# Kernel tuning notes

Measured on AMD Instinct MI355X. Metric: run time of the kernel, lower is better.

The kernel has to match this reference:

```python
import jax, jax.numpy as jnp
import numpy as np

ALPHA = 0.2  # leaky_relu negative slope
NEG_INF = -9e15


def gat_layer(h_in, W, a, adj_mask):
    """One GATLayer (eval mode, dropout disabled).
    h_in: [N, F_in], W: [F_in, F_out], a: [2*F_out, 1], adj_mask: [N, N] bool.
    Equivalent to the torch repeat/cat construction: e_ij = leaky_relu(a1.h_i + a2.h_j).
    """
    h = h_in @ W                          # [N, F_out]
    F_out = W.shape[1]
    a1 = a[:F_out, 0]                     # [F_out]
    a2 = a[F_out:, 0]                     # [F_out]
    f1 = h @ a1                           # [N]
    f2 = h @ a2                           # [N]
    e = jax.nn.leaky_relu(f1[:, None] + f2[None, :], negative_slope=ALPHA)  # [N, N]
    e = jnp.where(adj_mask, e, NEG_INF)
    attn = jax.nn.softmax(e, axis=-1)     # rows sum to 1
    return jax.nn.elu(attn @ h)           # [N, F_out]


def setup_inputs() -> dict:
    key = jax.random.key(0)
    ks = jax.random.split(key, 6)
    N, F_in, F_hid, F_out, H = 8192, 29, 8, 2, 4
    x = jax.random.normal(ks[0], (N, F_in), dtype=jnp.float32)
    adj = jax.random.randint(ks[1], (N, N), 0, 2, dtype=jnp.int32)
    # xavier_uniform with gain=1.414
    def xavier(k, shape, gain=1.414):
        fan_in, fan_out = shape[0], shape[1]
        bound = gain * np.sqrt(6.0 / (fan_in + fan_out))
        return jax.random.uniform(k, shape, jnp.float32, -bound, bound)
    W_heads = jnp.stack([xavier(k, (F_in, F_hid)) for k in jax.random.split(ks[2], H)])   # [H, 29, 8]
    a_heads = jnp.stack([xavier(k, (2 * F_hid, 1)) for k in jax.random.split(ks[3], H)])  # [H, 16, 1]
    W_out = xavier(ks[4], (F_hid * H, F_out))   # [32, 2]
    a_out = xavier(ks[5], (2 * F_out, 1))       # [4, 1]
    return {"x": x, "adj": adj, "W_heads": W_heads, "a_heads": a_heads,
            "W_out": W_out, "a_out": a_out}


def reference(x, adj, W_heads, a_heads, W_out, a_out):
    adj_mask = adj > 0
    heads = jax.vmap(lambda W, a: gat_layer(x, W, a, adj_mask))(W_heads, a_heads)  # [H, N, 8]
    hcat = jnp.concatenate(list(heads), axis=1)   # [N, H*8] (same order as torch cat over heads)
    out = gat_layer(hcat, W_out, a_out, adj_mask)  # [N, 2]
    return jax.nn.log_softmax(out, axis=1)
```

## Files before the change

### kernel.cpp

```cpp
#include <hip/hip_runtime.h>
#include <math.h>

#define N 8192
#define NW 128
#define FIN 29
#define FH 8
#define NH 4
#define ALPHA 0.2f
#define LOG2E 1.4426950408889634f

typedef unsigned long long ull;

__device__ inline unsigned bf16rn(float f) {
    unsigned u = __float_as_uint(f);
    return (u + 0x7fffu + ((u >> 16) & 1u)) >> 16;
}
__device__ inline float2 bfpair(unsigned u) {
    return make_float2(__uint_as_float(u << 16), __uint_as_float(u & 0xffff0000u));
}
__device__ inline unsigned fenc(float x) {
    unsigned u = __float_as_uint(x);
    return (u & 0x80000000u) ? ~u : (u | 0x80000000u);
}
__device__ inline float fdec(unsigned e) {
    return __uint_as_float((e & 0x80000000u) ? (e & 0x7fffffffu) : ~e);
}

__global__ void k0_pack(const int* __restrict__ adj, ull* __restrict__ mask,
                        unsigned* __restrict__ amax) {
    int row = blockIdx.x;
    int tid = threadIdx.x;
    int lane = tid & 63;
    int wave = tid >> 6;
    if (row == 0 && tid < 8) amax[tid] = 0u;
    const int* rp = adj + (size_t)row * N;
#pragma unroll 8
    for (int i = 0; i < 32; i++) {
        int a = rp[i * 256 + tid];
        ull b = __ballot(a > 0);
        if (lane == 0) mask[(size_t)row * NW + i * 4 + wave] = b;
    }
}

__global__ __launch_bounds__(64) void k1_feat(
    const float* __restrict__ x, const float* __restrict__ Wh,
    const float* __restrict__ ah,
    float* __restrict__ f2p, uint4* __restrict__ hpk,
    float* __restrict__ f1a, unsigned* __restrict__ amax) {
    __shared__ float sW[NH * FIN * FH];
    __shared__ float sa[NH * 2 * FH];
    int tid = threadIdx.x;
    for (int i = tid; i < NH * FIN * FH; i += 64) sW[i] = Wh[i];
    for (int i = tid; i < NH * 2 * FH; i += 64) sa[i] = ah[i];
    __syncthreads();
    int node = blockIdx.x * 64 + tid;
    float xr[FIN];
#pragma unroll
    for (int f = 0; f < FIN; f++) xr[f] = x[node * FIN + f];
    float f2v[NH];
#pragma unroll
    for (int h = 0; h < NH; h++) {
        float hv[FH];
#pragma unroll
        for (int k = 0; k < FH; k++) {
            float s = 0.f;
#pragma unroll
            for (int f = 0; f < FIN; f++) s += xr[f] * sW[(h * FIN + f) * FH + k];
            hv[k] = s;
        }
        float f1 = 0.f, f2 = 0.f;
#pragma unroll
        for (int k = 0; k < FH; k++) {
            f1 += hv[k] * sa[h * 16 + k];
            f2 += hv[k] * sa[h * 16 + 8 + k];
        }
        f2v[h] = f2 * LOG2E;
        f2p[h * N + node] = f2v[h];
        f1a[node * 4 + h] = f1 * LOG2E;
        uint4 p;
        p.x = (bf16rn(hv[1]) << 16) | bf16rn(hv[0]);
        p.y = (bf16rn(hv[3]) << 16) | bf16rn(hv[2]);
        p.z = (bf16rn(hv[5]) << 16) | bf16rn(hv[4]);
        p.w = (bf16rn(hv[7]) << 16) | bf16rn(hv[6]);
        hpk[h * N + node] = p;
    }
#pragma unroll
    for (int h = 0; h < NH; h++) {
        float v = f2v[h];
        for (int off = 32; off > 0; off >>= 1) v = fmaxf(v, __shfl_xor(v, off, 64));
        if (tid == 0) atomicMax(&amax[h], fenc(v));
    }
}

#define TJ 512
#define JS1 2
__global__ __launch_bounds__(512) void k3_attn1(
    const ull* __restrict__ mask, const float* __restrict__ f2p,
    const uint4* __restrict__ hpk, const float* __restrict__ f1a,
    const unsigned* __restrict__ amax, float* __restrict__ part1) {
    __shared__ float tF2[TJ];
    __shared__ uint4 tH[TJ];
    int tid = threadIdx.x;
    int lane = tid & 63;
    int wave = tid >> 6;
    int h = blockIdx.x & 3;
    int js = (blockIdx.x >> 2) & (JS1 - 1);
    int rowblk = blockIdx.x >> 3;
    int r0 = rowblk * 16 + wave * 2;
    int r1 = r0 + 1;
    const int JR = N / JS1;
    int jbase = js * JR;

    float mf = fdec(amax[h]);
    float f1 = f1a[r0 * 4 + h];
    float v = f1 + mf, m = fmaxf(v, ALPHA * v);
    float f1m0 = f1 - m, f1q0 = ALPHA * f1 - m;
    f1 = f1a[r1 * 4 + h];
    v = f1 + mf; m = fmaxf(v, ALPHA * v);
    float f1m1 = f1 - m, f1q1 = ALPHA * f1 - m;

    float acc0[FH], acc1[FH], d0 = 0.f, d1 = 0.f;
#pragma unroll
    for (int k = 0; k < FH; k++) { acc0[k] = 0.f; acc1[k] = 0.f; }

    const ull* mr0 = mask + (size_t)r0 * NW;
    const ull* mr1 = mask + (size_t)r1 * NW;

    for (int t = 0; t < JR / TJ; t++) {
        __syncthreads();
        int gb = jbase + t * TJ + tid;
        tH[tid] = hpk[h * N + gb];
        tF2[tid] = f2p[h * N + gb];
        __syncthreads();
        int wb = (jbase >> 6) + t * (TJ / 64);
#pragma unroll
        for (int s = 0; s < TJ / 64; s++) {
            ull mw0 = mr0[wb + s];
            ull mw1 = mr1[wb + s];
            bool b0 = (mw0 >> lane) & 1ull;
            bool b1 = (mw1 >> lane) & 1ull;
            int jl = s * 64 + lane;
            float f2 = tF2[jl];
            uint4 hq = tH[jl];
            float2 hv01 = bfpair(hq.x);
            float2 hv23 = bfpair(hq.y);
            float2 hv45 = bfpair(hq.z);
            float2 hv67 = bfpair(hq.w);
            float p = ALPHA * f2;
            float w0 = __builtin_amdgcn_exp2f(fmaxf(f1m0 + f2, p + f1q0));
            w0 = b0 ? w0 : 0.f;
            float w1 = __builtin_amdgcn_exp2f(fmaxf(f1m1 + f2, p + f1q1));
            w1 = b1 ? w1 : 0.f;
            acc0[0] = fmaf(w0, hv01.x, acc0[0]);
            acc0[1] = fmaf(w0, hv01.y, acc0[1]);
            acc0[2] = fmaf(w0, hv23.x, acc0[2]);
            acc0[3] = fmaf(w0, hv23.y, acc0[3]);
            acc0[4] = fmaf(w0, hv45.x, acc0[4]);
            acc0[5] = fmaf(w0, hv45.y, acc0[5]);
            acc0[6] = fmaf(w0, hv67.x, acc0[6]);
            acc0[7] = fmaf(w0, hv67.y, acc0[7]);
            d0 += w0;
            acc1[0] = fmaf(w1, hv01.x, acc1[0]);
            acc1[1] = fmaf(w1, hv01.y, acc1[1]);
            acc1[2] = fmaf(w1, hv23.x, acc1[2]);
            acc1[3] = fmaf(w1, hv23.y, acc1[3]);
            acc1[4] = fmaf(w1, hv45.x, acc1[4]);
            acc1[5] = fmaf(w1, hv45.y, acc1[5]);
            acc1[6] = fmaf(w1, hv67.x, acc1[6]);
            acc1[7] = fmaf(w1, hv67.y, acc1[7]);
            d1 += w1;
        }
    }
#pragma unroll
    for (int k = 0; k < FH; k++) {
        for (int off = 32; off > 0; off >>= 1) {
            acc0[k] += __shfl_xor(acc0[k], off, 64);
            acc1[k] += __shfl_xor(acc1[k], off, 64);
        }
    }
    for (int off = 32; off > 0; off >>= 1) {
        d0 += __shfl_xor(d0, off, 64);
        d1 += __shfl_xor(d1, off, 64);
    }
    if (lane == 0) {
#pragma unroll
        for (int k = 0; k < FH; k++) {
            part1[(js * 36 + h * 9 + k) * N + r0] = acc0[k];
            part1[(js * 36 + h * 9 + k) * N + r1] = acc1[k];
        }
        part1[(js * 36 + h * 9 + 8) * N + r0] = d0;
        part1[(js * 36 + h * 9 + 8) * N + r1] = d1;
    }
}

__global__ void k3b_final(const float* __restrict__ part1, const float* __restrict__ Wo,
                          const float* __restrict__ ao,
                          float4* __restrict__ rec2, float* __restrict__ f1b,
                          unsigned* __restrict__ amax) {
    __shared__ float sW[64];
    __shared__ float sa[4];
    int tid = threadIdx.x;
    if (tid < 64) sW[tid] = Wo[tid];
    if (tid < 4) sa[tid] = ao[tid];
    __syncthreads();
    int row = blockIdx.x * 256 + tid;
    float hv[32];
#pragma unroll
    for (int h = 0; h < NH; h++) {
        float s[9];
#pragma unroll
        for (int c = 0; c < 9; c++)
            s[c] = part1[(h * 9 + c) * N + row] + part1[(36 + h * 9 + c) * N + row];
        float inv = 1.f / s[8];
#pragma unroll
        for (int k = 0; k < FH; k++) {
            float o = s[k] * inv;
            hv[h * 8 + k] = (o > 0.f) ? o : expm1f(o);
        }
    }
    float h0 = 0.f, h1 = 0.f;
#pragma unroll
    for (int i = 0; i < 32; i++) {
        h0 = fmaf(hv[i], sW[i * 2 + 0], h0);
        h1 = fmaf(hv[i], sW[i * 2 + 1], h1);
    }
    float f1 = (h0 * sa[0] + h1 * sa[1]) * LOG2E;
    float f2 = (h0 * sa[2] + h1 * sa[3]) * LOG2E;
    rec2[row] = make_float4(f2, h0, h1, 0.f);
    f1b[row] = f1;
    float vmax = f2;
    for (int off = 32; off > 0; off >>= 1) vmax = fmaxf(vmax, __shfl_xor(vmax, off, 64));
    if ((tid & 63) == 0) atomicMax(&amax[4], fenc(vmax));
}

#define JS2 4
__global__ __launch_bounds__(256) void k6_attn2(
    const ull* __restrict__ mask, const float4* __restrict__ rec2,
    const float* __restrict__ f1b, const unsigned* __restrict__ amax,
    float* __restrict__ part2) {
    int tid = threadIdx.x;
    int lane = tid & 63;
    int wave = tid >> 6;
    int blk = blockIdx.x >> 2;
    int js = blockIdx.x & 3;
    int rbase = blk * 16 + wave * 4;
    const int JR = N / JS2;
    int jbase = js * JR;

    float mb = fdec(amax[4]);
    float f1m[4], f1q[4];
#pragma unroll
    for (int i = 0; i < 4; i++) {
        float f1 = f1b[rbase + i];
        float v = f1 + mb, m = fmaxf(v, ALPHA * v);
        f1m[i] = f1 - m; f1q[i] = ALPHA * f1 - m;
    }
    float a0[4] = {0.f, 0.f, 0.f, 0.f};
    float a1[4] = {0.f, 0.f, 0.f, 0.f};
    float dd[4] = {0.f, 0.f, 0.f, 0.f};
    const ull* mr[4];
#pragma unroll
    for (int i = 0; i < 4; i++) mr[i] = mask + (size_t)(rbase + i) * NW;

    int wb = jbase >> 6;
#pragma unroll 4
    for (int s = 0; s < JR / 64; s++) {
        float4 q = rec2[jbase + s * 64 + lane];
        float p = ALPHA * q.x;
#pragma unroll
        for (int i = 0; i < 4; i++) {
            ull mw = mr[i][wb + s];
            float w = __builtin_amdgcn_exp2f(fmaxf(f1m[i] + q.x, p + f1q[i]));
            w = ((mw >> lane) & 1ull) ? w : 0.f;
            a0[i] = fmaf(w, q.y, a0[i]);
            a1[i] = fmaf(w, q.z, a1[i]);
            dd[i] += w;
        }
    }
#pragma unroll
    for (int i = 0; i < 4; i++) {
        for (int off = 32; off > 0; off >>= 1) {
            a0[i] += __shfl_xor(a0[i], off, 64);
            a1[i] += __shfl_xor(a1[i], off, 64);
            dd[i] += __shfl_xor(dd[i], off, 64);
        }
    }
    if (lane == 0) {
#pragma unroll
        for (int i = 0; i < 4; i++) {
            int row = rbase + i;
            part2[(js * 3 + 0) * N + row] = a0[i];
            part2[(js * 3 + 1) * N + row] = a1[i];
            part2[(js * 3 + 2) * N + row] = dd[i];
        }
    }
}

__global__ void k6b_final(const float* __restrict__ part2, float* __restrict__ out) {
    int row = blockIdx.x * 256 + threadIdx.x;
    float s0 = 0.f, s1 = 0.f, d = 0.f;
#pragma unroll
    for (int js = 0; js < JS2; js++) {
        s0 += part2[(js * 3 + 0) * N + row];
        s1 += part2[(js * 3 + 1) * N + row];
        d  += part2[(js * 3 + 2) * N + row];
    }
    float inv = 1.f / d;
    float e0 = s0 * inv, e1 = s1 * inv;
    e0 = (e0 > 0.f) ? e0 : expm1f(e0);
    e1 = (e1 > 0.f) ? e1 : expm1f(e1);
    float mx = fmaxf(e0, e1);
    float lse = mx + logf(expf(e0 - mx) + expf(e1 - mx));
    ((float2*)out)[row] = make_float2(e0 - lse, e1 - lse);
}

extern "C" void kernel_launch(void* const* d_in, const int* in_sizes, int n_in,
                              void* d_out, int out_size, void* d_ws, size_t ws_size,
                              hipStream_t stream) {
    const float* x   = (const float*)d_in[0];
    const int*   adj = (const int*)d_in[1];
    const float* Wh  = (const float*)d_in[2];
    const float* ah  = (const float*)d_in[3];
    const float* Wo  = (const float*)d_in[4];
    const float* ao  = (const float*)d_in[5];
    float* out = (float*)d_out;
    float* ws = (float*)d_ws;

    ull*      mask  = (ull*)ws;
    float*    f2p   = ws + 2097152;
    uint4*    hpk   = (uint4*)(ws + 2129920);
    float*    f1a   = ws + 2260992;
    float*    part1 = ws + 2293760;
    float4*   rec2  = (float4*)(ws + 2883584);
    float*    f1b   = ws + 2916352;
    float*    part2 = ws + 2924544;
    unsigned* amax  = (unsigned*)(ws + 3022848);

    k0_pack<<<N, 256, 0, stream>>>(adj, mask, amax);
    k1_feat<<<N / 64, 64, 0, stream>>>(x, Wh, ah, f2p, hpk, f1a, amax);
    k3_attn1<<<(N / 16) * JS1 * NH, 512, 0, stream>>>(mask, f2p, hpk, f1a, amax, part1);
    k3b_final<<<N / 256, 256, 0, stream>>>(part1, Wo, ao, rec2, f1b, amax);
    k6_attn2<<<(N / 16) * JS2, 256, 0, stream>>>(mask, rec2, f1b, amax, part2);
    k6b_final<<<N / 256, 256, 0, stream>>>(part2, out);
}
```

Baseline: 618.8 us.

## Factor attention exp into precomputed terms, widen row tiling, fuse final stage

```diff
diff --git a/kernel.cpp b/kernel.cpp
--- a/kernel.cpp
+++ b/kernel.cpp
@@ -24,6 +24,14 @@
 }
 __device__ inline float fdec(unsigned e) {
     return __uint_as_float((e & 0x80000000u) ? (e & 0x7fffffffu) : ~e);
+}
+__device__ inline float selmask(float w, ull mw) {
+    unsigned lo = __builtin_amdgcn_readfirstlane((unsigned)mw);
+    unsigned hi = __builtin_amdgcn_readfirstlane((unsigned)(mw >> 32));
+    ull smw = ((ull)hi << 32) | lo;
+    float r;
+    asm("v_cndmask_b32 %0, 0, %1, %2" : "=v"(r) : "v"(w), "s"(smw));
+    return r;
 }
 
 __global__ void k0_pack(const int* __restrict__ adj, ull* __restrict__ mask,
@@ -45,7 +53,7 @@
 __global__ __launch_bounds__(64) void k1_feat(
     const float* __restrict__ x, const float* __restrict__ Wh,
     const float* __restrict__ ah,
-    float* __restrict__ f2p, uint4* __restrict__ hpk,
+    float4* __restrict__ tup1, uint4* __restrict__ hpk,
     float* __restrict__ f1a, unsigned* __restrict__ amax) {
     __shared__ float sW[NH * FIN * FH];
     __shared__ float sa[NH * 2 * FH];
@@ -74,8 +82,11 @@
             f1 += hv[k] * sa[h * 16 + k];
             f2 += hv[k] * sa[h * 16 + 8 + k];
         }
-        f2v[h] = f2 * LOG2E;
-        f2p[h * N + node] = f2v[h];
+        float f2s = f2 * LOG2E;
+        f2v[h] = f2s;
+        tup1[h * N + node] = make_float4(f2s,
+                                         __builtin_amdgcn_exp2f(f2s),
+                                         __builtin_amdgcn_exp2f(ALPHA * f2s), 0.f);
         f1a[node * 4 + h] = f1 * LOG2E;
         uint4 p;
         p.x = (bf16rn(hv[1]) << 16) | bf16rn(hv[0]);
@@ -95,10 +106,10 @@
 #define TJ 512
 #define JS1 2
 __global__ __launch_bounds__(512) void k3_attn1(
-    const ull* __restrict__ mask, const float* __restrict__ f2p,
+    const ull* __restrict__ mask, const float4* __restrict__ tup1,
     const uint4* __restrict__ hpk, const float* __restrict__ f1a,
     const unsigned* __restrict__ amax, float* __restrict__ part1) {
-    __shared__ float tF2[TJ];
+    __shared__ float4 tT[TJ];
     __shared__ uint4 tH[TJ];
     int tid = threadIdx.x;
     int lane = tid & 63;
@@ -106,90 +117,92 @@
     int h = blockIdx.x & 3;
     int js = (blockIdx.x >> 2) & (JS1 - 1);
     int rowblk = blockIdx.x >> 3;
-    int r0 = rowblk * 16 + wave * 2;
-    int r1 = r0 + 1;
+    int r0 = rowblk * 32 + wave * 4;
     const int JR = N / JS1;
     int jbase = js * JR;
 
     float mf = fdec(amax[h]);
-    float f1 = f1a[r0 * 4 + h];
-    float v = f1 + mf, m = fmaxf(v, ALPHA * v);
-    float f1m0 = f1 - m, f1q0 = ALPHA * f1 - m;
-    f1 = f1a[r1 * 4 + h];
-    v = f1 + mf; m = fmaxf(v, ALPHA * v);
-    float f1m1 = f1 - m, f1q1 = ALPHA * f1 - m;
-
-    float acc0[FH], acc1[FH], d0 = 0.f, d1 = 0.f;
-#pragma unroll
-    for (int k = 0; k < FH; k++) { acc0[k] = 0.f; acc1[k] = 0.f; }
-
-    const ull* mr0 = mask + (size_t)r0 * NW;
-    const ull* mr1 = mask + (size_t)r1 * NW;
+    float f1r[4], C1[4], C2[4];
+#pragma unroll
+    for (int r = 0; r < 4; r++) {
+        float f1 = f1a[(r0 + r) * 4 + h];
+        float v = f1 + mf, m = fmaxf(v, ALPHA * v);
+        f1r[r] = f1;
+        C1[r] = __builtin_amdgcn_exp2f(f1 - m);
+        C2[r] = __builtin_amdgcn_exp2f(ALPHA * f1 - m);
+    }
+    float2 acc[4][4];
+    float dsum[4];
+#pragma unroll
+    for (int r = 0; r < 4; r++) {
+        dsum[r] = 0.f;
+#pragma unroll
+        for (int k = 0; k < 4; k++) acc[r][k] = make_float2(0.f, 0.f);
+    }
+    const ull* mr[4];
+#pragma unroll
+    for (int r = 0; r < 4; r++) mr[r] = mask + (size_t)(r0 + r) * NW;
 
     for (int t = 0; t < JR / TJ; t++) {
         __syncthreads();
         int gb = jbase + t * TJ + tid;
+        tT[tid] = tup1[h * N + gb];
         tH[tid] = hpk[h * N + gb];
-        tF2[tid] = f2p[h * N + gb];
         __syncthreads();
         int wb = (jbase >> 6) + t * (TJ / 64);
 #pragma unroll
         for (int s = 0; s < TJ / 64; s++) {
-            ull mw0 = mr0[wb + s];
-            ull mw1 = mr1[wb + s];
-            bool b0 = (mw0 >> lane) & 1ull;
-            bool b1 = (mw1 >> lane) & 1ull;
+            ull mw[4];
+#pragma unroll
+            for (int r = 0; r < 4; r++) mw[r] = mr[r][wb + s];
             int jl = s * 64 + lane;
-            float f2 = tF2[jl];
+            float4 tq = tT[jl];
             uint4 hq = tH[jl];
             float2 hv01 = bfpair(hq.x);
             float2 hv23 = bfpair(hq.y);
             float2 hv45 = bfpair(hq.z);
             float2 hv67 = bfpair(hq.w);
-            float p = ALPHA * f2;
-            float w0 = __builtin_amdgcn_exp2f(fmaxf(f1m0 + f2, p + f1q0));
-            w0 = b0 ? w0 : 0.f;
-            float w1 = __builtin_amdgcn_exp2f(fmaxf(f1m1 + f2, p + f1q1));
-            w1 = b1 ? w1 : 0.f;
-            acc0[0] = fmaf(w0, hv01.x, acc0[0]);
-            acc0[1] = fmaf(w0, hv01.y, acc0[1]);
-            acc0[2] = fmaf(w0, hv23.x, acc0[2]);
-            acc0[3] = fmaf(w0, hv23.y, acc0[3]);
-            acc0[4] = fmaf(w0, hv45.x, acc0[4]);
-            acc0[5] = fmaf(w0, hv45.y, acc0[5]);
-            acc0[6] = fmaf(w0, hv67.x, acc0[6]);
-            acc0[7] = fmaf(w0, hv67.y, acc0[7]);
-            d0 += w0;
-            acc1[0] = fmaf(w1, hv01.x, acc1[0]);
-            acc1[1] = fmaf(w1, hv01.y, acc1[1]);
-            acc1[2] = fmaf(w1, hv23.x, acc1[2]);
-            acc1[3] = fmaf(w1, hv23.y, acc1[3]);
-            acc1[4] = fmaf(w1, hv45.x, acc1[4]);
-            acc1[5] = fmaf(w1, hv45.y, acc1[5]);
-            acc1[6] = fmaf(w1, hv67.x, acc1[6]);
-            acc1[7] = fmaf(w1, hv67.y, acc1[7]);
-            d1 += w1;
-        }
-    }
-#pragma unroll
-    for (int k = 0; k < FH; k++) {
-        for (int off = 32; off > 0; off >>= 1) {
-            acc0[k] += __shfl_xor(acc0[k], off, 64);
-            acc1[k] += __shfl_xor(acc1[k], off, 64);
-        }
-    }
-    for (int off = 32; off > 0; off >>= 1) {
-        d0 += __shfl_xor(d0, off, 64);
-        d1 += __shfl_xor(d1, off, 64);
+#pragma unroll
+            for (int r = 0; r < 4; r++) {
+                float sg = f1r[r] + tq.x;
+                float E = (sg >= 0.f) ? tq.y : tq.z;
+                float C = (sg >= 0.f) ? C1[r] : C2[r];
+                float w = selmask(C * E, mw[r]);
+                acc[r][0].x = fmaf(w, hv01.x, acc[r][0].x);
+                acc[r][0].y = fmaf(w, hv01.y, acc[r][0].y);
+                acc[r][1].x = fmaf(w, hv23.x, acc[r][1].x);
+                acc[r][1].y = fmaf(w, hv23.y, acc[r][1].y);
+                acc[r][2].x = fmaf(w, hv45.x, acc[r][2].x);
+                acc[r][2].y = fmaf(w, hv45.y, acc[r][2].y);
+                acc[r][3].x = fmaf(w, hv67.x, acc[r][3].x);
+                acc[r][3].y = fmaf(w, hv67.y, acc[r][3].y);
+                dsum[r] += w;
+            }
+        }
+    }
+#pragma unroll
+    for (int r = 0; r < 4; r++) {
+#pragma unroll
+        for (int k = 0; k < 4; k++) {
+            for (int off = 32; off > 0; off >>= 1) {
+                acc[r][k].x += __shfl_xor(acc[r][k].x, off, 64);
+                acc[r][k].y += __shfl_xor(acc[r][k].y, off, 64);
+            }
+        }
+        for (int off = 32; off > 0; off >>= 1)
+            dsum[r] += __shfl_xor(dsum[r], off, 64);
     }
     if (lane == 0) {
 #pragma unroll
-        for (int k = 0; k < FH; k++) {
-            part1[(js * 36 + h * 9 + k) * N + r0] = acc0[k];
-            part1[(js * 36 + h * 9 + k) * N + r1] = acc1[k];
-        }
-        part1[(js * 36 + h * 9 + 8) * N + r0] = d0;
-        part1[(js * 36 + h * 9 + 8) * N + r1] = d1;
+        for (int r = 0; r < 4; r++) {
+            int row = r0 + r;
+#pragma unroll
+            for (int k = 0; k < 4; k++) {
+                part1[(js * 36 + h * 9 + 2 * k + 0) * N + row] = acc[r][k].x;
+                part1[(js * 36 + h * 9 + 2 * k + 1) * N + row] = acc[r][k].y;
+            }
+            part1[(js * 36 + h * 9 + 8) * N + row] = dsum[r];
+        }
     }
 }
 
@@ -233,19 +246,14 @@
     if ((tid & 63) == 0) atomicMax(&amax[4], fenc(vmax));
 }
 
-#define JS2 4
 __global__ __launch_bounds__(256) void k6_attn2(
     const ull* __restrict__ mask, const float4* __restrict__ rec2,
     const float* __restrict__ f1b, const unsigned* __restrict__ amax,
-    float* __restrict__ part2) {
+    float* __restrict__ out) {
     int tid = threadIdx.x;
     int lane = tid & 63;
     int wave = tid >> 6;
-    int blk = blockIdx.x >> 2;
-    int js = blockIdx.x & 3;
-    int rbase = blk * 16 + wave * 4;
-    const int JR = N / JS2;
-    int jbase = js * JR;
+    int rbase = blockIdx.x * 16 + wave * 4;
 
     float mb = fdec(amax[4]);
     float f1m[4], f1q[4];
@@ -262,16 +270,15 @@
 #pragma unroll
     for (int i = 0; i < 4; i++) mr[i] = mask + (size_t)(rbase + i) * NW;
 
-    int wb = jbase >> 6;
 #pragma unroll 4
-    for (int s = 0; s < JR / 64; s++) {
-        float4 q = rec2[jbase + s * 64 + lane];
+    for (int s = 0; s < N / 64; s++) {
+        float4 q = rec2[s * 64 + lane];
         float p = ALPHA * q.x;
 #pragma unroll
         for (int i = 0; i < 4; i++) {
-            ull mw = mr[i][wb + s];
+            ull mw = mr[i][s];
             float w = __builtin_amdgcn_exp2f(fmaxf(f1m[i] + q.x, p + f1q[i]));
-            w = ((mw >> lane) & 1ull) ? w : 0.f;
+            w = selmask(w, mw);
             a0[i] = fmaf(w, q.y, a0[i]);
             a1[i] = fmaf(w, q.z, a1[i]);
             dd[i] += w;
@@ -288,30 +295,15 @@
     if (lane == 0) {
 #pragma unroll
         for (int i = 0; i < 4; i++) {
-            int row = rbase + i;
-            part2[(js * 3 + 0) * N + row] = a0[i];
-            part2[(js * 3 + 1) * N + row] = a1[i];
-            part2[(js * 3 + 2) * N + row] = dd[i];
-        }
-    }
-}
-
-__global__ void k6b_final(const float* __restrict__ part2, float* __restrict__ out) {
-    int row = blockIdx.x * 256 + threadIdx.x;
-    float s0 = 0.f, s1 = 0.f, d = 0.f;
-#pragma unroll
-    for (int js = 0; js < JS2; js++) {
-        s0 += part2[(js * 3 + 0) * N + row];
-        s1 += part2[(js * 3 + 1) * N + row];
-        d  += part2[(js * 3 + 2) * N + row];
-    }
-    float inv = 1.f / d;
-    float e0 = s0 * inv, e1 = s1 * inv;
-    e0 = (e0 > 0.f) ? e0 : expm1f(e0);
-    e1 = (e1 > 0.f) ? e1 : expm1f(e1);
-    float mx = fmaxf(e0, e1);
-    float lse = mx + logf(expf(e0 - mx) + expf(e1 - mx));
-    ((float2*)out)[row] = make_float2(e0 - lse, e1 - lse);
+            float inv = 1.f / dd[i];
+            float e0 = a0[i] * inv, e1 = a1[i] * inv;
+            e0 = (e0 > 0.f) ? e0 : expm1f(e0);
+            e1 = (e1 > 0.f) ? e1 : expm1f(e1);
+            float mx = fmaxf(e0, e1);
+            float lse = mx + logf(expf(e0 - mx) + expf(e1 - mx));
+            ((float2*)out)[rbase + i] = make_float2(e0 - lse, e1 - lse);
+        }
+    }
 }
 
 extern "C" void kernel_launch(void* const* d_in, const int* in_sizes, int n_in,
@@ -327,19 +319,17 @@
     float* ws = (float*)d_ws;
 
     ull*      mask  = (ull*)ws;
-    float*    f2p   = ws + 2097152;
-    uint4*    hpk   = (uint4*)(ws + 2129920);
-    float*    f1a   = ws + 2260992;
-    float*    part1 = ws + 2293760;
-    float4*   rec2  = (float4*)(ws + 2883584);
-    float*    f1b   = ws + 2916352;
-    float*    part2 = ws + 2924544;
+    float4*   tup1  = (float4*)(ws + 2097152);
+    uint4*    hpk   = (uint4*)(ws + 2228224);
+    float*    f1a   = ws + 2359296;
+    float*    part1 = ws + 2392064;
+    float4*   rec2  = (float4*)(ws + 2981888);
+    float*    f1b   = ws + 3014656;
     unsigned* amax  = (unsigned*)(ws + 3022848);
 
     k0_pack<<<N, 256, 0, stream>>>(adj, mask, amax);
-    k1_feat<<<N / 64, 64, 0, stream>>>(x, Wh, ah, f2p, hpk, f1a, amax);
-    k3_attn1<<<(N / 16) * JS1 * NH, 512, 0, stream>>>(mask, f2p, hpk, f1a, amax, part1);
+    k1_feat<<<N / 64, 64, 0, stream>>>(x, Wh, ah, tup1, hpk, f1a, amax);
+    k3_attn1<<<(N / 32) * JS1 * NH, 512, 0, stream>>>(mask, tup1, hpk, f1a, amax, part1);
     k3b_final<<<N / 256, 256, 0, stream>>>(part1, Wo, ao, rec2, f1b, amax);
-    k6_attn2<<<(N / 16) * JS2, 256, 0, stream>>>(mask, rec2, f1b, amax, part2);
-    k6b_final<<<N / 256, 256, 0, stream>>>(part2, out);
-}
+    k6_attn2<<<N / 16, 256, 0, stream>>>(mask, rec2, f1b, amax, out);
+}
```

Measured after the change: 626.2 us. About the same (+1.2%).
